# Optimization experiments

Measured on AMD Instinct MI355X. Metric: run time of the kernel, lower is better.

Reference implementation:

```python
import jax, jax.numpy as jnp
import numpy as np

STRIDE = 4
IMG_H, IMG_W = 800, 1216
NMS_THRESH = 0.7
PRE_NMS = 1000
POST_NMS = 1000
MIN_SIZE = 0.0
SCALE_CLAMP = float(np.log(1000.0 / 16.0))  # detectron2 Box2BoxTransform clamp
A = 3  # anchors per location


def _cell_anchors():
    size = 32.0
    ars = jnp.array([0.5, 1.0, 2.0], jnp.float32)
    area = size * size
    w = jnp.sqrt(area / ars)
    h = ars * w
    return jnp.stack([-w / 2, -h / 2, w / 2, h / 2], axis=1)  # [A,4]


def _anchors(H, W):
    sx = jnp.arange(W, dtype=jnp.float32) * STRIDE
    sy = jnp.arange(H, dtype=jnp.float32) * STRIDE
    gy, gx = jnp.meshgrid(sy, sx, indexing='ij')
    shifts = jnp.stack([gx, gy, gx, gy], axis=-1).reshape(-1, 1, 4)  # [H*W,1,4]
    return (shifts + _cell_anchors()[None]).reshape(-1, 4)  # [H*W*A,4]


def _conv(x, w, b, pad):
    y = jax.lax.conv_general_dilated(x, w, (1, 1), pad,
                                     dimension_numbers=('NCHW', 'OIHW', 'NCHW'))
    return y + b[None, :, None, None]


def _decode(anchors, deltas):
    # anchors [M,4], deltas [N,M,4]; weights (1,1,1,1)
    wa = anchors[:, 2] - anchors[:, 0]
    ha = anchors[:, 3] - anchors[:, 1]
    cx = anchors[:, 0] + 0.5 * wa
    cy = anchors[:, 1] + 0.5 * ha
    dx, dy = deltas[..., 0], deltas[..., 1]
    dw = jnp.minimum(deltas[..., 2], SCALE_CLAMP)
    dh = jnp.minimum(deltas[..., 3], SCALE_CLAMP)
    px = dx * wa + cx
    py = dy * ha + cy
    pw = jnp.exp(dw) * wa
    ph = jnp.exp(dh) * ha
    return jnp.stack([px - 0.5 * pw, py - 0.5 * ph,
                      px + 0.5 * pw, py + 0.5 * ph], axis=-1)


def _iou_matrix(boxes):  # [K,4] -> [K,K]
    area = (boxes[:, 2] - boxes[:, 0]) * (boxes[:, 3] - boxes[:, 1])
    lt = jnp.maximum(boxes[:, None, :2], boxes[None, :, :2])
    rb = jnp.minimum(boxes[:, None, 2:], boxes[None, :, 2:])
    wh = jnp.clip(rb - lt, 0.0)
    inter = wh[..., 0] * wh[..., 1]
    return inter / jnp.maximum(area[:, None] + area[None, :] - inter, 1e-9)


def _nms_keep(boxes):
    # boxes already sorted by descending score; greedy NMS
    iou = _iou_matrix(boxes)
    K = boxes.shape[0]

    def step(sup, i):
        keep = ~sup[i]
        sup = sup | (keep & (iou[i] > NMS_THRESH))
        return sup, keep

    _, keep = jax.lax.scan(step, jnp.zeros(K, bool), jnp.arange(K))
    return keep


def setup_inputs() -> dict:
    key = jax.random.key(0)
    ks = jax.random.split(key, 4)
    features = jax.random.normal(ks[0], (2, 256, 200, 304), jnp.float32)
    w_conv = jax.random.normal(ks[1], (256, 256, 3, 3), jnp.float32) * 0.01
    b_conv = jnp.zeros((256,), jnp.float32)
    w_obj = jax.random.normal(ks[2], (3, 256, 1, 1), jnp.float32) * 0.01
    b_obj = jnp.zeros((3,), jnp.float32)
    w_delta = jax.random.normal(ks[3], (12, 256, 1, 1), jnp.float32) * 0.01
    b_delta = jnp.zeros((12,), jnp.float32)
    return {"features": features, "w_conv": w_conv, "b_conv": b_conv,
            "w_obj": w_obj, "b_obj": b_obj, "w_delta": w_delta, "b_delta": b_delta}


def reference(features, w_conv, b_conv, w_obj, b_obj, w_delta, b_delta):
    N, C, H, W = features.shape
    t = jax.nn.relu(_conv(features, w_conv, b_conv, 'SAME'))
    logits = _conv(t, w_obj, b_obj, 'VALID')            # [N,A,H,W]
    deltas = _conv(t, w_delta, b_delta, 'VALID')        # [N,4A,H,W]
    logits = logits.transpose(0, 2, 3, 1).reshape(N, -1)               # [N,H*W*A]
    deltas = deltas.reshape(N, A, 4, H, W).transpose(0, 3, 4, 1, 2).reshape(N, -1, 4)

    anchors = _anchors(H, W)                             # [H*W*A,4]
    boxes = _decode(anchors, deltas)                     # [N,M,4]
    boxes = jnp.stack([jnp.clip(boxes[..., 0], 0.0, IMG_W),
                       jnp.clip(boxes[..., 1], 0.0, IMG_H),
                       jnp.clip(boxes[..., 2], 0.0, IMG_W),
                       jnp.clip(boxes[..., 3], 0.0, IMG_H)], axis=-1)

    valid = ((boxes[..., 2] - boxes[..., 0]) >= MIN_SIZE) & \
            ((boxes[..., 3] - boxes[..., 1]) >= MIN_SIZE)
    scores = jnp.where(valid, logits, -jnp.inf)

    top_s, top_i = jax.lax.top_k(scores, PRE_NMS)                      # sorted desc
    top_b = jnp.take_along_axis(boxes, top_i[..., None], axis=1)       # [N,K,4]

    keep = jax.vmap(_nms_keep)(top_b)                                  # [N,K]
    s = jnp.where(keep, top_s, -jnp.inf)
    fin_s, fin_i = jax.lax.top_k(s, POST_NMS)                          # sorted desc (=final sort)
    fin_b = jnp.take_along_axis(top_b, fin_i[..., None], axis=1)
    fin_b = jnp.where(jnp.isfinite(fin_s)[..., None], fin_b, 0.0)
    return fin_b, fin_s
```

## Files before the change

### kernel.cpp

```cpp
#include <hip/hip_runtime.h>
#include <math.h>
#include <stdint.h>

#define CC 256
#define HH 200
#define WW 304
#define NN 2
#define HW 60800
#define MM 182400
#define KK 1000
#define HP 202
#define WP 306
#define SCALE_CLAMP_F 4.135166556742356f
#define NEG_SENTINEL -1.0e30f
#define CAND_CAP 4096

typedef __attribute__((ext_vector_type(8))) short short8;
typedef __attribute__((ext_vector_type(4))) float f32x4;

__device__ __forceinline__ unsigned short f2bf(float f) {
  unsigned u = __float_as_uint(f);
  u += 0x7FFFu + ((u >> 16) & 1u);
  return (unsigned short)(u >> 16);
}
__device__ __forceinline__ unsigned int fkey(float s) {
  unsigned int u = __float_as_uint(s);
  return (u & 0x80000000u) ? ~u : (u | 0x80000000u);
}
__device__ __forceinline__ float iou_ref(float4 a, float4 b) {
#pragma clang fp contract(off)
  float areaA = (a.z - a.x) * (a.w - a.y);
  float areaB = (b.z - b.x) * (b.w - b.y);
  float ltx = fmaxf(a.x, b.x), lty = fmaxf(a.y, b.y);
  float rbx = fminf(a.z, b.z), rby = fminf(a.w, b.w);
  float w = fmaxf(rbx - ltx, 0.0f), h = fmaxf(rby - lty, 0.0f);
  float inter = w * h;
  float denom = fmaxf(areaA + areaB - inter, 1e-9f);
  return inter / denom;
}
__device__ __forceinline__ void gload16(const void* g, void* l) {
  __builtin_amdgcn_global_load_lds(
      (const __attribute__((address_space(1))) unsigned int*)g,
      (__attribute__((address_space(3))) unsigned int*)l, 16, 0, 0);
}
__device__ __forceinline__ int swz(int byte) {
  return byte ^ (((byte >> 7) & 7) << 4);
}

__global__ __launch_bounds__(256) void wt_pack(const float* __restrict__ w,
                                               unsigned short* __restrict__ wt_b) {
  int o = blockIdx.x * 256 + threadIdx.x;
  int cin = o & 255, cout = (o >> 8) & 255, pos = o >> 16;
  wt_b[o] = f2bf(w[(cout * 256 + cin) * 9 + pos]);
}

__global__ __launch_bounds__(256) void in_pack(const float* __restrict__ in,
                                               unsigned short* __restrict__ fbp) {
  __shared__ unsigned short tile[64][65];
  int tid = threadIdx.x;
  int p0 = blockIdx.x * 64;
  int c0 = blockIdx.y * 64;
  int n = blockIdx.z;
  int lane = tid & 63;
  int p = p0 + lane;
  int yp = 0, xp = 0;
  bool inb = false;
  if (p < HP * WP) {
    yp = p / WP; xp = p - yp * WP;
    inb = (yp >= 1 && yp <= HH && xp >= 1 && xp <= WW);
  }
  for (int ci = tid >> 6; ci < 64; ci += 4) {
    float v = 0.f;
    if (inb) v = in[(((size_t)n * CC + c0 + ci) * HH + (yp - 1)) * WW + (xp - 1)];
    tile[ci][lane] = f2bf(v);
  }
  __syncthreads();
  for (int i = 0; i < 4; ++i) {
    int idx4 = (i * 256 + tid) * 4;
    int hwi = idx4 >> 6, cb = idx4 & 63;
    int pp = p0 + hwi;
    if (pp < HP * WP) {
      ushort4 v;
      v.x = tile[cb][hwi]; v.y = tile[cb + 1][hwi];
      v.z = tile[cb + 2][hwi]; v.w = tile[cb + 3][hwi];
      *(ushort4*)&fbp[((size_t)n * HP * WP + pp) * 256 + c0 + cb] = v;
    }
  }
}

__global__ __launch_bounds__(512) void conv_mfma(
    const unsigned short* __restrict__ wt_b, const unsigned short* __restrict__ fbp,
    const float* __restrict__ bias, const float* __restrict__ w_obj,
    const float* __restrict__ b_obj, const float* __restrict__ w_delta,
    const float* __restrict__ b_delta, float* __restrict__ scores,
    float* __restrict__ boxes, unsigned long long* __restrict__ keys) {
  __shared__ __align__(16) unsigned short lA[2][8192];
  __shared__ __align__(16) unsigned short lB[2][5760];
  __shared__ float whl[4096];
  __shared__ float bl[256];
  int tid = threadIdx.x;
  int lane = tid & 63, wid = tid >> 6;
  int wm = wid >> 1, wn = wid & 1;
  int lrow = lane & 15, lgrp = lane >> 4;
  int n = blockIdx.z;
  int X0 = blockIdx.x * 16, Y0 = blockIdx.y * 8;

  f32x4 acc[4][4];
#pragma unroll
  for (int m = 0; m < 4; ++m)
#pragma unroll
    for (int r = 0; r < 4; ++r) acc[m][r] = {0.f, 0.f, 0.f, 0.f};

  int wbase = wid << 10;

  auto stageA = [&](int pos, int cc, int buf) {
#pragma unroll
    for (int is = 0; is < 2; ++is) {
      int idx = is * 512 + tid;
      int L = swz(idx * 16);
      int cout = L >> 6, q = (L >> 4) & 3;
      const unsigned short* g = wt_b + (((size_t)pos * 256 + cout) << 8) + cc * 32 + q * 8;
      gload16(g, (char*)&lA[buf][0] + is * 8192 + wbase);
    }
  };
  auto stageB = [&](int cc, int buf) {
#pragma unroll
    for (int is = 0; is < 2; ++is) {
      int idx = is * 512 + tid;
      if (idx < 720) {
        int L = swz(idx * 16);
        int rc = L >> 6, q = (L >> 4) & 3;
        int row = rc / 18, col = rc - row * 18;
        const unsigned short* g =
            fbp + (((size_t)n * HP + Y0 + row) * WP + X0 + col) * 256 + cc * 32 + q * 8;
        gload16(g, (char*)&lB[buf][0] + is * 8192 + wbase);
      }
    }
  };

  for (int i = tid; i < 4096; i += 512) {
    int c = i >> 4, o = i & 15;
    float v = 0.f;
    if (o < 3) v = w_obj[o * 256 + c];
    else if (o < 15) v = w_delta[(o - 3) * 256 + c];
    whl[i] = v;
  }
  if (tid < 256) bl[tid] = bias[tid];

  stageA(0, 0, 0);
  stageB(0, 0);
  __syncthreads();

  int ab = 0;
#pragma unroll 1
  for (int cc = 0; cc < 8; ++cc) {
    int bb = cc & 1;
#pragma unroll
    for (int pos = 0; pos < 9; ++pos) {
      if (pos < 8) stageA(pos + 1, cc, ab ^ 1);
      else if (cc < 7) stageA(0, cc + 1, ab ^ 1);
      if (pos == 0 && cc < 7) stageB(cc + 1, bb ^ 1);
      int ky = pos / 3, kx = pos - ky * 3;
      short8 af[4], bfr[4];
#pragma unroll
      for (int m = 0; m < 4; ++m) {
        int Lb = ((wm * 64 + m * 16 + lrow) << 6) + (lgrp << 4);
        af[m] = *(const short8*)((const char*)&lA[ab][0] + swz(Lb));
      }
#pragma unroll
      for (int r = 0; r < 4; ++r) {
        int Lb = (((wn * 4 + r + ky) * 18 + lrow + kx) << 6) + (lgrp << 4);
        bfr[r] = *(const short8*)((const char*)&lB[bb][0] + swz(Lb));
      }
#pragma unroll
      for (int m = 0; m < 4; ++m)
#pragma unroll
        for (int r = 0; r < 4; ++r)
          acc[m][r] = __builtin_amdgcn_mfma_f32_16x16x32_bf16(af[m], bfr[r], acc[m][r], 0, 0, 0);
      __syncthreads();
      ab ^= 1;
    }
  }

#pragma unroll
  for (int m = 0; m < 4; ++m)
#pragma unroll
    for (int j = 0; j < 4; ++j) {
      int cout = wm * 64 + m * 16 + (lgrp << 2) + j;
      float b = bl[cout];
#pragma unroll
      for (int r = 0; r < 4; ++r) acc[m][r][j] = fmaxf(acc[m][r][j] + b, 0.f);
    }

  float* hacc = (float*)&lA[0][0];
#pragma unroll 1
  for (int o = 0; o < 15; ++o) {
    float p0 = 0.f, p1 = 0.f, p2 = 0.f, p3 = 0.f;
#pragma unroll
    for (int m = 0; m < 4; ++m)
#pragma unroll
      for (int j = 0; j < 4; ++j) {
        float w = whl[((wm * 64 + m * 16 + (lgrp << 2) + j) << 4) + o];
        p0 = fmaf(w, acc[m][0][j], p0);
        p1 = fmaf(w, acc[m][1][j], p1);
        p2 = fmaf(w, acc[m][2][j], p2);
        p3 = fmaf(w, acc[m][3][j], p3);
      }
    p0 += __shfl_xor(p0, 16); p0 += __shfl_xor(p0, 32);
    p1 += __shfl_xor(p1, 16); p1 += __shfl_xor(p1, 32);
    p2 += __shfl_xor(p2, 16); p2 += __shfl_xor(p2, 32);
    p3 += __shfl_xor(p3, 16); p3 += __shfl_xor(p3, 32);
    if (lgrp == 0) {
      hacc[(((o * 8) + wn * 4 + 0) * 16 + lrow) * 4 + wm] = p0;
      hacc[(((o * 8) + wn * 4 + 1) * 16 + lrow) * 4 + wm] = p1;
      hacc[(((o * 8) + wn * 4 + 2) * 16 + lrow) * 4 + wm] = p2;
      hacc[(((o * 8) + wn * 4 + 3) * 16 + lrow) * 4 + wm] = p3;
    }
  }
  __syncthreads();

  if (tid < 128) {
    int row = tid >> 4, col = tid & 15;
    int y = Y0 + row, x = X0 + col;
    float hv[15];
#pragma unroll
    for (int o = 0; o < 15; ++o) {
      const float* hp = &hacc[((o * 8 + row) * 16 + col) * 4];
      hv[o] = ((hp[0] + hp[1]) + hp[2]) + hp[3];
    }
    float ho[15];
#pragma unroll
    for (int o = 0; o < 3; ++o) ho[o] = hv[o] + b_obj[o];
#pragma unroll
    for (int o = 0; o < 12; ++o) ho[3 + o] = hv[3 + o] + b_delta[o];
    {
#pragma clang fp contract(off)
      int loc = y * WW + x;
      float gx = (float)(x * 4);
      float gy = (float)(y * 4);
      float s2048 = sqrtf(2048.0f), s512 = sqrtf(512.0f);
      float aw[3] = {s2048, 32.0f, s512};
      float ah[3] = {0.5f * s2048, 32.0f, 2.0f * s512};
#pragma unroll
      for (int a = 0; a < 3; ++a) {
        float ax1 = gx - 0.5f * aw[a], ay1 = gy - 0.5f * ah[a];
        float ax2 = gx + 0.5f * aw[a], ay2 = gy + 0.5f * ah[a];
        float wa = ax2 - ax1, ha = ay2 - ay1;
        float cx = ax1 + 0.5f * wa, cy = ay1 + 0.5f * ha;
        float dx = ho[3 + a * 4 + 0], dy = ho[3 + a * 4 + 1];
        float dw = fminf(ho[3 + a * 4 + 2], SCALE_CLAMP_F);
        float dh = fminf(ho[3 + a * 4 + 3], SCALE_CLAMP_F);
        float px = dx * wa + cx, py = dy * ha + cy;
        float pw = expf(dw) * wa, ph = expf(dh) * ha;
        float x1 = px - 0.5f * pw, y1 = py - 0.5f * ph;
        float y2v = py + 0.5f * ph, x2v = px + 0.5f * pw;
        x1 = fminf(fmaxf(x1, 0.f), 1216.f);
        y1 = fminf(fmaxf(y1, 0.f), 800.f);
        x2v = fminf(fmaxf(x2v, 0.f), 1216.f);
        y2v = fminf(fmaxf(y2v, 0.f), 800.f);
        int m = loc * 3 + a;
        ((float4*)boxes)[(size_t)n * MM + m] = make_float4(x1, y1, x2v, y2v);
        float sc = ho[a];
        scores[(size_t)n * MM + m] = sc;
        keys[(size_t)n * MM + m] =
            ((unsigned long long)fkey(sc) << 18) | (unsigned long long)(262143 - m);
      }
    }
  }
}

__global__ __launch_bounds__(256) void zero_hist(unsigned int* __restrict__ ghist,
                                                 unsigned int* __restrict__ cnt) {
  int i = blockIdx.x * 256 + threadIdx.x;
  if (i < 2 * 8192) ghist[i] = 0;
  if (i < 2) cnt[i] = 0;
}

__global__ __launch_bounds__(256) void hist_kernel(const unsigned long long* __restrict__ keys,
                                                   unsigned int* __restrict__ ghist) {
  __shared__ unsigned int h[8192];
  int tid = threadIdx.x, n = blockIdx.y;
  for (int i = tid; i < 8192; i += 256) h[i] = 0;
  __syncthreads();
  const unsigned long long* kp = keys + (size_t)n * MM;
  int i0 = blockIdx.x * 2850, i1 = min(i0 + 2850, MM);
  for (int i = i0 + tid; i < i1; i += 256)
    atomicAdd(&h[(unsigned)(kp[i] >> 37)], 1u);
  __syncthreads();
  for (int i = tid; i < 8192; i += 256)
    if (h[i]) atomicAdd(&ghist[n * 8192 + i], h[i]);
}

__global__ __launch_bounds__(256) void pick_kernel(const unsigned int* __restrict__ ghist,
                                                   int* __restrict__ thrbin) {
  int n = blockIdx.x, tid = threadIdx.x;
  __shared__ unsigned int ps[256];
  const unsigned int* h = ghist + n * 8192;
  unsigned s = 0;
  for (int k = 0; k < 32; ++k) s += h[tid * 32 + k];
  ps[tid] = s;
  __syncthreads();
  if (tid == 0) {
    unsigned cum = 0; int b = 0;
    for (int t = 255; t >= 0; --t) {
      if (cum + ps[t] >= KK) {
        for (int bin = t * 32 + 31; bin >= t * 32; --bin) {
          cum += h[bin];
          if (cum >= KK) { b = bin; break; }
        }
        break;
      }
      cum += ps[t];
    }
    thrbin[n] = b;
  }
}

__global__ __launch_bounds__(256) void gather_kernel(
    const unsigned long long* __restrict__ keys, const int* __restrict__ thrbin,
    unsigned int* __restrict__ cnt, unsigned long long* __restrict__ cand) {
  int n = blockIdx.y;
  int b = thrbin[n];
  const unsigned long long* kp = keys + (size_t)n * MM;
  int i0 = blockIdx.x * 2850, i1 = min(i0 + 2850, MM);
  for (int i = i0 + threadIdx.x; i < i1; i += 256) {
    unsigned long long k = kp[i];
    if ((int)(unsigned)(k >> 37) >= b) {
      unsigned pos = atomicAdd(&cnt[n], 1u);
      if (pos < CAND_CAP) cand[(size_t)n * CAND_CAP + pos] = k;
    }
  }
}

__global__ __launch_bounds__(1024) void final_select(
    const unsigned long long* __restrict__ cand, const unsigned int* __restrict__ cnt,
    const float* __restrict__ scores, const float* __restrict__ boxes,
    float* __restrict__ s_scores, float* __restrict__ s_boxes) {
  __shared__ unsigned long long sel[CAND_CAP];
  int n = blockIdx.x, tid = threadIdx.x;
  int E = (int)min(cnt[n], (unsigned)CAND_CAP);
  for (int i = tid; i < CAND_CAP; i += 1024)
    sel[i] = (i < E) ? cand[(size_t)n * CAND_CAP + i] : 0ull;
  __syncthreads();
  for (unsigned k2 = 2; k2 <= CAND_CAP; k2 <<= 1) {
    for (unsigned j = k2 >> 1; j > 0; j >>= 1) {
      for (int i = tid; i < CAND_CAP; i += 1024) {
        int l = i ^ (int)j;
        if (l > i) {
          unsigned long long a = sel[i], bb = sel[l];
          bool sw = ((i & k2) == 0) ? (a < bb) : (a > bb);
          if (sw) { sel[i] = bb; sel[l] = a; }
        }
      }
      __syncthreads();
    }
  }
  if (tid < KK) {
    unsigned long long k = sel[tid];
    int m = 262143 - (int)(k & 0x3FFFFull);
    s_scores[n * KK + tid] = scores[(size_t)n * MM + m];
    ((float4*)s_boxes)[n * KK + tid] = ((const float4*)boxes)[(size_t)n * MM + m];
  }
}

__global__ __launch_bounds__(256) void mask_kernel(const float* __restrict__ s_boxes,
                                                   unsigned long long* __restrict__ mask) {
  int i = blockIdx.x, n = blockIdx.y;
  int tid = threadIdx.x, w = tid >> 6, lane = tid & 63;
  const float4* bp = (const float4*)s_boxes + n * KK;
  float4 bi = bp[i];
#pragma unroll
  for (int p = 0; p < 4; ++p) {
    int word = p * 4 + w;
    int j = word * 64 + lane;
    bool over = false;
    if (j < KK) {
      float4 bj = bp[j];
      over = iou_ref(bi, bj) > 0.7f;
    }
    unsigned long long bal = __ballot(over);
    if (lane == 0) mask[((size_t)n * KK + i) * 16 + word] = bal;
  }
}

__global__ __launch_bounds__(1024) void scan_write_kernel(
    const float* __restrict__ s_scores, const float* __restrict__ s_boxes,
    const unsigned long long* __restrict__ mask, float* __restrict__ out) {
  int n = blockIdx.x, tid = threadIdx.x;
  int wid = tid >> 6, lane = tid & 63;
  __shared__ unsigned long long swl[16];
  __shared__ unsigned long long keepw[16];
  __shared__ unsigned int wpre[17];
  if (tid < 16) swl[tid] = 0ull;
  __syncthreads();
  const unsigned long long* mrow = mask + (size_t)n * 16000;
  for (int c = 0; c < 16; ++c) {
    int i = c * 64 + lane;
    unsigned long long myword = (i < KK) ? mrow[(size_t)i * 16 + wid] : 0ull;
    if (wid == 0) {
      unsigned long long m = (i < KK) ? mrow[(size_t)i * 16 + c] : 0ull;
      unsigned long long cur = swl[c];
      unsigned long long kw = 0ull;
      int lim = min(64, KK - c * 64);
      for (int b = 0; b < lim; ++b) {
        unsigned long long mb = __shfl(m, b);
        if (!((cur >> b) & 1ull)) { kw |= (1ull << b); cur |= mb; }
      }
      if (lane == 0) keepw[c] = kw;
    }
    __syncthreads();
    unsigned long long kw = keepw[c];
    unsigned long long v = ((kw >> lane) & 1ull) ? myword : 0ull;
#pragma unroll
    for (int s = 32; s > 0; s >>= 1) v |= __shfl_xor(v, s);
    if (lane == 0) swl[wid] |= v;
    __syncthreads();
  }
  if (tid == 0) {
    unsigned int c = 0;
    for (int w2 = 0; w2 < 16; ++w2) { wpre[w2] = c; c += (unsigned int)__popcll(keepw[w2]); }
    wpre[16] = c;
  }
  __syncthreads();
  if (tid < KK) {
    int word = tid >> 6, bit = tid & 63;
    unsigned long long kwv = keepw[word];
    bool kept = (kwv >> bit) & 1ull;
    unsigned int before = wpre[word] + (unsigned int)__popcll(kwv & ((1ull << bit) - 1ull));
    unsigned int nk = wpre[16];
    unsigned int dst = kept ? before : nk + ((unsigned int)tid - before);
    float4 b = kept ? ((const float4*)s_boxes)[n * KK + tid] : make_float4(0.f, 0.f, 0.f, 0.f);
    float s = kept ? s_scores[n * KK + tid] : NEG_SENTINEL;
    ((float4*)out)[n * KK + dst] = b;
    out[8000 + n * KK + dst] = s;
  }
}

extern "C" void kernel_launch(void* const* d_in, const int* in_sizes, int n_in,
                              void* d_out, int out_size, void* d_ws, size_t ws_size,
                              hipStream_t stream) {
  (void)in_sizes; (void)n_in; (void)out_size; (void)ws_size;
  const float* features = (const float*)d_in[0];
  const float* w_conv   = (const float*)d_in[1];
  const float* b_conv   = (const float*)d_in[2];
  const float* w_obj    = (const float*)d_in[3];
  const float* b_obj    = (const float*)d_in[4];
  const float* w_delta  = (const float*)d_in[5];
  const float* b_delta  = (const float*)d_in[6];

  char* ws = (char*)d_ws;
  unsigned short* wt_b = (unsigned short*)ws;
  unsigned short* fbp  = (unsigned short*)(ws + 1179648);
  char* O = ws + 1179648 + 63295488;
  float* scores = (float*)O;
  float* boxes  = (float*)(O + 1459200);
  unsigned long long* keys = (unsigned long long*)(O + 7296000);
  char* P = O + 10214400;
  unsigned int* ghist = (unsigned int*)P;
  int* thrbin = (int*)(P + 65536);
  unsigned int* cnt = (unsigned int*)(P + 65792);
  unsigned long long* cand = (unsigned long long*)(P + 66048);
  float* s_scores = (float*)(P + 131584);
  float* s_boxes  = (float*)(P + 139776);
  unsigned long long* maskbuf = (unsigned long long*)(P + 172032);
  float* out = (float*)d_out;

  wt_pack<<<2304, 256, 0, stream>>>(w_conv, wt_b);
  in_pack<<<dim3(966, 4, 2), 256, 0, stream>>>(features, fbp);
  conv_mfma<<<dim3(19, 25, 2), 512, 0, stream>>>(wt_b, fbp, b_conv, w_obj, b_obj,
                                                 w_delta, b_delta, scores, boxes, keys);
  zero_hist<<<64, 256, 0, stream>>>(ghist, cnt);
  hist_kernel<<<dim3(64, 2), 256, 0, stream>>>(keys, ghist);
  pick_kernel<<<2, 256, 0, stream>>>(ghist, thrbin);
  gather_kernel<<<dim3(64, 2), 256, 0, stream>>>(keys, thrbin, cnt, cand);
  final_select<<<2, 1024, 0, stream>>>(cand, cnt, scores, boxes, s_scores, s_boxes);
  mask_kernel<<<dim3(1000, 2), 256, 0, stream>>>(s_boxes, maskbuf);
  scan_write_kernel<<<2, 1024, 0, stream>>>(s_scores, s_boxes, maskbuf, out);
}
```

Baseline: 448.5 us.

## Split conv output channels across two blocks and move decode to separate kernel

The 3x3 conv kernel now splits its 256 output channels into two halves, one per block. Each block runs 256 threads with less LDS, which doubles the grid to 1900 blocks and raises occupancy on the CUs. Each half writes partial 1x1-head sums to a global buffer, and a new decode kernel adds the two halves, applies the biases and decodes the boxes. The cost is an extra launch, a global round trip for the partial heads, and the 3x3 input tile being loaded twice. The candidate cap is also reduced and the workspace offsets are adjusted to match.

New measurement: 569.9 us. 1.27x slower.

```diff
diff --git a/kernel.cpp b/kernel.cpp
--- a/kernel.cpp
+++ b/kernel.cpp
@@ -13,7 +13,7 @@
 #define WP 306
 #define SCALE_CLAMP_F 4.135166556742356f
 #define NEG_SENTINEL -1.0e30f
-#define CAND_CAP 4096
+#define CAND_CAP 2048
 
 typedef __attribute__((ext_vector_type(8))) short short8;
 typedef __attribute__((ext_vector_type(4))) float f32x4;
@@ -88,21 +88,19 @@
   }
 }
 
-__global__ __launch_bounds__(512) void conv_mfma(
+__global__ __launch_bounds__(256, 4) void conv_mfma(
     const unsigned short* __restrict__ wt_b, const unsigned short* __restrict__ fbp,
     const float* __restrict__ bias, const float* __restrict__ w_obj,
-    const float* __restrict__ b_obj, const float* __restrict__ w_delta,
-    const float* __restrict__ b_delta, float* __restrict__ scores,
-    float* __restrict__ boxes, unsigned long long* __restrict__ keys) {
-  __shared__ __align__(16) unsigned short lA[2][8192];
+    const float* __restrict__ w_delta, float* __restrict__ phead) {
+  __shared__ __align__(16) unsigned short lA[2][4096];
   __shared__ __align__(16) unsigned short lB[2][5760];
-  __shared__ float whl[4096];
-  __shared__ float bl[256];
+  __shared__ float bl_l[128];
   int tid = threadIdx.x;
   int lane = tid & 63, wid = tid >> 6;
   int wm = wid >> 1, wn = wid & 1;
   int lrow = lane & 15, lgrp = lane >> 4;
-  int n = blockIdx.z;
+  int zz = blockIdx.z;
+  int n = zz >> 1, ct = zz & 1;
   int X0 = blockIdx.x * 16, Y0 = blockIdx.y * 8;
 
   f32x4 acc[4][4];
@@ -111,41 +109,33 @@
 #pragma unroll
     for (int r = 0; r < 4; ++r) acc[m][r] = {0.f, 0.f, 0.f, 0.f};
 
-  int wbase = wid << 10;
+  if (tid < 128) bl_l[tid] = bias[ct * 128 + tid];
 
   auto stageA = [&](int pos, int cc, int buf) {
 #pragma unroll
     for (int is = 0; is < 2; ++is) {
-      int idx = is * 512 + tid;
+      int idx = is * 256 + tid;
       int L = swz(idx * 16);
       int cout = L >> 6, q = (L >> 4) & 3;
-      const unsigned short* g = wt_b + (((size_t)pos * 256 + cout) << 8) + cc * 32 + q * 8;
-      gload16(g, (char*)&lA[buf][0] + is * 8192 + wbase);
+      const unsigned short* g =
+          wt_b + (((size_t)pos * 256 + ct * 128 + cout) << 8) + cc * 32 + q * 8;
+      gload16(g, (char*)&lA[buf][0] + is * 4096 + (wid << 10));
     }
   };
   auto stageB = [&](int cc, int buf) {
 #pragma unroll
-    for (int is = 0; is < 2; ++is) {
-      int idx = is * 512 + tid;
+    for (int is = 0; is < 3; ++is) {
+      int idx = is * 256 + tid;
       if (idx < 720) {
         int L = swz(idx * 16);
         int rc = L >> 6, q = (L >> 4) & 3;
         int row = rc / 18, col = rc - row * 18;
         const unsigned short* g =
             fbp + (((size_t)n * HP + Y0 + row) * WP + X0 + col) * 256 + cc * 32 + q * 8;
-        gload16(g, (char*)&lB[buf][0] + is * 8192 + wbase);
+        gload16(g, (char*)&lB[buf][0] + is * 4096 + (wid << 10));
       }
     }
   };
-
-  for (int i = tid; i < 4096; i += 512) {
-    int c = i >> 4, o = i & 15;
-    float v = 0.f;
-    if (o < 3) v = w_obj[o * 256 + c];
-    else if (o < 15) v = w_delta[(o - 3) * 256 + c];
-    whl[i] = v;
-  }
-  if (tid < 256) bl[tid] = bias[tid];
 
   stageA(0, 0, 0);
   stageB(0, 0);
@@ -186,13 +176,20 @@
   for (int m = 0; m < 4; ++m)
 #pragma unroll
     for (int j = 0; j < 4; ++j) {
-      int cout = wm * 64 + m * 16 + (lgrp << 2) + j;
-      float b = bl[cout];
+      float b = bl_l[wm * 64 + m * 16 + (lgrp << 2) + j];
 #pragma unroll
       for (int r = 0; r < 4; ++r) acc[m][r][j] = fmaxf(acc[m][r][j] + b, 0.f);
     }
 
-  float* hacc = (float*)&lA[0][0];
+  float* whl_l = (float*)&lA[0][0];
+  for (int i = tid; i < 1920; i += 256) {
+    int o = i >> 7, cl = i & 127;
+    whl_l[i] = (o < 3) ? w_obj[o * 256 + ct * 128 + cl]
+                       : w_delta[(o - 3) * 256 + ct * 128 + cl];
+  }
+  __syncthreads();
+
+  float* hacc = (float*)&lB[0][0];
 #pragma unroll 1
   for (int o = 0; o < 15; ++o) {
     float p0 = 0.f, p1 = 0.f, p2 = 0.f, p3 = 0.f;
@@ -200,7 +197,7 @@
     for (int m = 0; m < 4; ++m)
 #pragma unroll
       for (int j = 0; j < 4; ++j) {
-        float w = whl[((wm * 64 + m * 16 + (lgrp << 2) + j) << 4) + o];
+        float w = whl_l[o * 128 + wm * 64 + m * 16 + (lgrp << 2) + j];
         p0 = fmaf(w, acc[m][0][j], p0);
         p1 = fmaf(w, acc[m][1][j], p1);
         p2 = fmaf(w, acc[m][2][j], p2);
@@ -211,60 +208,73 @@
     p2 += __shfl_xor(p2, 16); p2 += __shfl_xor(p2, 32);
     p3 += __shfl_xor(p3, 16); p3 += __shfl_xor(p3, 32);
     if (lgrp == 0) {
-      hacc[(((o * 8) + wn * 4 + 0) * 16 + lrow) * 4 + wm] = p0;
-      hacc[(((o * 8) + wn * 4 + 1) * 16 + lrow) * 4 + wm] = p1;
-      hacc[(((o * 8) + wn * 4 + 2) * 16 + lrow) * 4 + wm] = p2;
-      hacc[(((o * 8) + wn * 4 + 3) * 16 + lrow) * 4 + wm] = p3;
+      hacc[(((o * 8) + wn * 4 + 0) * 16 + lrow) * 2 + wm] = p0;
+      hacc[(((o * 8) + wn * 4 + 1) * 16 + lrow) * 2 + wm] = p1;
+      hacc[(((o * 8) + wn * 4 + 2) * 16 + lrow) * 2 + wm] = p2;
+      hacc[(((o * 8) + wn * 4 + 3) * 16 + lrow) * 2 + wm] = p3;
     }
   }
   __syncthreads();
 
   if (tid < 128) {
     int row = tid >> 4, col = tid & 15;
-    int y = Y0 + row, x = X0 + col;
-    float hv[15];
+    int loc = (Y0 + row) * WW + (X0 + col);
+    size_t base = ((size_t)zz * 15) * HW + loc;
 #pragma unroll
     for (int o = 0; o < 15; ++o) {
-      const float* hp = &hacc[((o * 8 + row) * 16 + col) * 4];
-      hv[o] = ((hp[0] + hp[1]) + hp[2]) + hp[3];
-    }
-    float ho[15];
-#pragma unroll
-    for (int o = 0; o < 3; ++o) ho[o] = hv[o] + b_obj[o];
-#pragma unroll
-    for (int o = 0; o < 12; ++o) ho[3 + o] = hv[3 + o] + b_delta[o];
-    {
+      const float* hp = &hacc[((o * 8 + row) * 16 + col) * 2];
+      phead[base + (size_t)o * HW] = hp[0] + hp[1];
+    }
+  }
+}
+
+__global__ __launch_bounds__(256) void decode_kernel(
+    const float* __restrict__ phead, const float* __restrict__ b_obj,
+    const float* __restrict__ b_delta, float* __restrict__ scores,
+    float* __restrict__ boxes, unsigned long long* __restrict__ keys) {
+  int n = blockIdx.y;
+  int loc = blockIdx.x * 256 + threadIdx.x;
+  if (loc >= HW) return;
+  float ho[15];
+  const float* p0 = phead + ((size_t)(n * 2 + 0) * 15) * HW + loc;
+  const float* p1 = phead + ((size_t)(n * 2 + 1) * 15) * HW + loc;
+#pragma unroll
+  for (int o = 0; o < 15; ++o) ho[o] = p0[(size_t)o * HW] + p1[(size_t)o * HW];
+#pragma unroll
+  for (int o = 0; o < 3; ++o) ho[o] += b_obj[o];
+#pragma unroll
+  for (int o = 0; o < 12; ++o) ho[3 + o] += b_delta[o];
+  {
 #pragma clang fp contract(off)
-      int loc = y * WW + x;
-      float gx = (float)(x * 4);
-      float gy = (float)(y * 4);
-      float s2048 = sqrtf(2048.0f), s512 = sqrtf(512.0f);
-      float aw[3] = {s2048, 32.0f, s512};
-      float ah[3] = {0.5f * s2048, 32.0f, 2.0f * s512};
-#pragma unroll
-      for (int a = 0; a < 3; ++a) {
-        float ax1 = gx - 0.5f * aw[a], ay1 = gy - 0.5f * ah[a];
-        float ax2 = gx + 0.5f * aw[a], ay2 = gy + 0.5f * ah[a];
-        float wa = ax2 - ax1, ha = ay2 - ay1;
-        float cx = ax1 + 0.5f * wa, cy = ay1 + 0.5f * ha;
-        float dx = ho[3 + a * 4 + 0], dy = ho[3 + a * 4 + 1];
-        float dw = fminf(ho[3 + a * 4 + 2], SCALE_CLAMP_F);
-        float dh = fminf(ho[3 + a * 4 + 3], SCALE_CLAMP_F);
-        float px = dx * wa + cx, py = dy * ha + cy;
-        float pw = expf(dw) * wa, ph = expf(dh) * ha;
-        float x1 = px - 0.5f * pw, y1 = py - 0.5f * ph;
-        float y2v = py + 0.5f * ph, x2v = px + 0.5f * pw;
-        x1 = fminf(fmaxf(x1, 0.f), 1216.f);
-        y1 = fminf(fmaxf(y1, 0.f), 800.f);
-        x2v = fminf(fmaxf(x2v, 0.f), 1216.f);
-        y2v = fminf(fmaxf(y2v, 0.f), 800.f);
-        int m = loc * 3 + a;
-        ((float4*)boxes)[(size_t)n * MM + m] = make_float4(x1, y1, x2v, y2v);
-        float sc = ho[a];
-        scores[(size_t)n * MM + m] = sc;
-        keys[(size_t)n * MM + m] =
-            ((unsigned long long)fkey(sc) << 18) | (unsigned long long)(262143 - m);
-      }
+    int h = loc / WW, w = loc - h * WW;
+    float gx = (float)(w * 4);
+    float gy = (float)(h * 4);
+    float s2048 = sqrtf(2048.0f), s512 = sqrtf(512.0f);
+    float aw[3] = {s2048, 32.0f, s512};
+    float ah[3] = {0.5f * s2048, 32.0f, 2.0f * s512};
+#pragma unroll
+    for (int a = 0; a < 3; ++a) {
+      float ax1 = gx - 0.5f * aw[a], ay1 = gy - 0.5f * ah[a];
+      float ax2 = gx + 0.5f * aw[a], ay2 = gy + 0.5f * ah[a];
+      float wa = ax2 - ax1, ha = ay2 - ay1;
+      float cx = ax1 + 0.5f * wa, cy = ay1 + 0.5f * ha;
+      float dx = ho[3 + a * 4 + 0], dy = ho[3 + a * 4 + 1];
+      float dw = fminf(ho[3 + a * 4 + 2], SCALE_CLAMP_F);
+      float dh = fminf(ho[3 + a * 4 + 3], SCALE_CLAMP_F);
+      float px = dx * wa + cx, py = dy * ha + cy;
+      float pw = expf(dw) * wa, ph = expf(dh) * ha;
+      float x1 = px - 0.5f * pw, y1 = py - 0.5f * ph;
+      float x2v = px + 0.5f * pw, y2v = py + 0.5f * ph;
+      x1 = fminf(fmaxf(x1, 0.f), 1216.f);
+      y1 = fminf(fmaxf(y1, 0.f), 800.f);
+      x2v = fminf(fmaxf(x2v, 0.f), 1216.f);
+      y2v = fminf(fmaxf(y2v, 0.f), 800.f);
+      int m = loc * 3 + a;
+      ((float4*)boxes)[(size_t)n * MM + m] = make_float4(x1, y1, x2v, y2v);
+      float sc = ho[a];
+      scores[(size_t)n * MM + m] = sc;
+      keys[(size_t)n * MM + m] =
+          ((unsigned long long)fkey(sc) << 18) | (unsigned long long)(262143 - m);
     }
   }
 }
@@ -451,24 +461,26 @@
   char* ws = (char*)d_ws;
   unsigned short* wt_b = (unsigned short*)ws;
   unsigned short* fbp  = (unsigned short*)(ws + 1179648);
-  char* O = ws + 1179648 + 63295488;
-  float* scores = (float*)O;
-  float* boxes  = (float*)(O + 1459200);
-  unsigned long long* keys = (unsigned long long*)(O + 7296000);
-  char* P = O + 10214400;
+  char* O = ws + 64475136;
+  float* phead = (float*)O;
+  float* scores = (float*)(O + 14592000);
+  float* boxes  = (float*)(O + 16051200);
+  unsigned long long* keys = (unsigned long long*)(O + 21888000);
+  char* P = O + 24806400;
   unsigned int* ghist = (unsigned int*)P;
   int* thrbin = (int*)(P + 65536);
   unsigned int* cnt = (unsigned int*)(P + 65792);
   unsigned long long* cand = (unsigned long long*)(P + 66048);
-  float* s_scores = (float*)(P + 131584);
-  float* s_boxes  = (float*)(P + 139776);
-  unsigned long long* maskbuf = (unsigned long long*)(P + 172032);
+  float* s_scores = (float*)(P + 98816);
+  float* s_boxes  = (float*)(P + 107008);
+  unsigned long long* maskbuf = (unsigned long long*)(P + 139264);
   float* out = (float*)d_out;
 
   wt_pack<<<2304, 256, 0, stream>>>(w_conv, wt_b);
   in_pack<<<dim3(966, 4, 2), 256, 0, stream>>>(features, fbp);
-  conv_mfma<<<dim3(19, 25, 2), 512, 0, stream>>>(wt_b, fbp, b_conv, w_obj, b_obj,
-                                                 w_delta, b_delta, scores, boxes, keys);
+  conv_mfma<<<dim3(19, 25, 4), 256, 0, stream>>>(wt_b, fbp, b_conv, w_obj, w_delta, phead);
+  decode_kernel<<<dim3(238, 2), 256, 0, stream>>>(phead, b_obj, b_delta,
+                                                  scores, boxes, keys);
   zero_hist<<<64, 256, 0, stream>>>(ghist, cnt);
   hist_kernel<<<dim3(64, 2), 256, 0, stream>>>(keys, ghist);
   pick_kernel<<<2, 256, 0, stream>>>(ghist, thrbin);
```
